# Kernel optimization log

Hardware: AMD Instinct MI355X
Metric: run time of the kernel (lower is better)

## Reference

```python
import jax, jax.numpy as jnp
import numpy as np

B, H, S, D = 4, 16, 2048, 128

def setup_inputs() -> dict:
    key = jax.random.key(0)
    kk, kq, kv = jax.random.split(key, 3)
    k = jax.random.normal(kk, (B, H, S, D), dtype=jnp.float32)
    q = jax.random.normal(kq, (B, H, S, D), dtype=jnp.float32)
    v = jax.random.normal(kv, (B, H, S, D), dtype=jnp.float32)
    # causal mask: True = masked out (strictly upper triangle)
    mask = jnp.triu(jnp.ones((S, S), dtype=bool), k=1)
    return {"k": k, "q": q, "v": v, "mask": mask}

def reference(k, q, v, mask):
    d_k = k.shape[-1]
    # scores: [B, H, S, S]
    scores = jnp.einsum("bhqd,bhkd->bhqk", q, k) / jnp.sqrt(jnp.asarray(d_k, q.dtype))
    scores = jnp.where(mask, -jnp.inf, scores)
    # numerically stable softmax over last dim (matches manual max/exp/sum)
    p = jax.nn.softmax(scores, axis=-1)
    return jnp.einsum("bhqk,bhkd->bhqd", p, v)
```

## Files before the change

kernel.cpp:

```cpp
#include <hip/hip_runtime.h>
#include <hip/hip_bf16.h>
#include <math.h>

#define BATCH 4
#define HEADS 16
#define SEQ   2048
#define DIM   128
#define BHN   (BATCH*HEADS)

#define BQ 128
#define WQ 32
#define KT 32
#define NXB (SEQ/BQ)

typedef short bf16x8 __attribute__((ext_vector_type(8)));
typedef float f32x4  __attribute__((ext_vector_type(4)));

static __device__ __forceinline__ unsigned short f2bf(float f) {
    union { float f; unsigned u; } x; x.f = f;
    unsigned r = x.u + 0x7FFF + ((x.u >> 16) & 1);
    return (unsigned short)(r >> 16);
}

static __device__ __forceinline__ void async_cp16(const unsigned short* g, unsigned short* l) {
    __builtin_amdgcn_global_load_lds(
        (const __attribute__((address_space(1))) unsigned int*)g,
        (__attribute__((address_space(3))) unsigned int*)l,
        16, 0, 0);
}

__global__ __launch_bounds__(256) void cvt_kv(
    const float* __restrict__ k, const float* __restrict__ v,
    unsigned short* __restrict__ kb, unsigned short* __restrict__ vt) {
    __shared__ unsigned short T[DIM][72];
    const int bh = blockIdx.y;
    const int s0 = blockIdx.x * 64;
    const int t  = threadIdx.x;
    const long rbase = ((long)bh * SEQ + s0) * DIM;

    #pragma unroll
    for (int u = 0; u < 2; ++u) {
        long e = rbase + (long)(t + u * 256) * 16;
        const float* src = k + e;
        unsigned short* dst = kb + e;
        #pragma unroll
        for (int h = 0; h < 2; ++h) {
            float4 a0 = *(const float4*)(src + h * 8);
            float4 a1 = *(const float4*)(src + h * 8 + 4);
            union { uint4 u4; unsigned short s[8]; } p;
            p.s[0]=f2bf(a0.x); p.s[1]=f2bf(a0.y); p.s[2]=f2bf(a0.z); p.s[3]=f2bf(a0.w);
            p.s[4]=f2bf(a1.x); p.s[5]=f2bf(a1.y); p.s[6]=f2bf(a1.z); p.s[7]=f2bf(a1.w);
            *(uint4*)(dst + h * 8) = p.u4;
        }
    }
    {
        const int r = t >> 2, i = t & 3;
        const float* src = v + rbase + (long)r * DIM + i * 32;
        #pragma unroll
        for (int j = 0; j < 8; ++j) {
            float4 x = *(const float4*)(src + j * 4);
            const int d = i * 32 + j * 4;
            T[d + 0][r] = f2bf(x.x); T[d + 1][r] = f2bf(x.y);
            T[d + 2][r] = f2bf(x.z); T[d + 3][r] = f2bf(x.w);
        }
    }
    __syncthreads();
    {
        const int d = t >> 1, h = t & 1;
        unsigned short* dst = vt + ((long)bh * DIM + d) * SEQ + s0 + h * 32;
        #pragma unroll
        for (int m = 0; m < 4; ++m)
            *(uint4*)(dst + m * 8) = *(const uint4*)&T[d][h * 32 + m * 8];
    }
}

__global__ __launch_bounds__(256, 2) void attn_fwd(
    const float* __restrict__ qg,
    const unsigned short* __restrict__ kb,
    const unsigned short* __restrict__ vtg,
    float* __restrict__ out) {

    __shared__ unsigned short Kt[2][KT][DIM];
    __shared__ unsigned short Vt[2][DIM][KT];
    __shared__ unsigned short Pl[4][2][16][KT + 8];

    const int tid  = threadIdx.x;
    const int w    = tid >> 6;
    const int lane = tid & 63;
    const int quad = lane >> 4;
    const int ql   = lane & 15;

    const int flat = blockIdx.x;
    const int xcd  = flat & 7;
    const int slot = flat >> 3;
    const int bh   = (xcd << 3) | (slot & 7);
    const int shi  = slot >> 3;
    const int xb   = (shi < 4) ? (15 - shi)
                   : (shi < 8) ? (shi - 4)
                   : (shi < 12) ? shi
                   : (19 - shi);
    const int qb0 = xb * BQ;
    const int qw0 = qb0 + w * WQ;

    const long base = (long)bh * SEQ * DIM;
    const float scale = 0.08838834764831845f * 1.4426950408889634f;

    bf16x8 qf[2][4];
    #pragma unroll
    for (int mb = 0; mb < 2; ++mb) {
        const float* qr = qg + base + (long)(qw0 + mb * 16 + ql) * DIM;
        #pragma unroll
        for (int c = 0; c < 4; ++c) {
            const float* p = qr + c * 32 + quad * 8;
            float4 x = *(const float4*)(p);
            float4 y = *(const float4*)(p + 4);
            union { bf16x8 v; unsigned short s[8]; } u;
            u.s[0]=f2bf(x.x*scale); u.s[1]=f2bf(x.y*scale);
            u.s[2]=f2bf(x.z*scale); u.s[3]=f2bf(x.w*scale);
            u.s[4]=f2bf(y.x*scale); u.s[5]=f2bf(y.y*scale);
            u.s[6]=f2bf(y.z*scale); u.s[7]=f2bf(y.w*scale);
            qf[mb][c] = u.v;
        }
    }

    f32x4 acc[2][8];
    #pragma unroll
    for (int mb = 0; mb < 2; ++mb)
        #pragma unroll
        for (int n = 0; n < 8; ++n)
            acc[mb][n] = (f32x4){0.f, 0.f, 0.f, 0.f};

    float m_[2] = {-INFINITY, -INFINITY};
    float l_[2] = {0.f, 0.f};

    auto stage = [&](int buf, int k0) {
        #pragma unroll
        for (int i = 0; i < 2; ++i) {
            const int idx = tid + i * 256;
            const int r   = idx >> 4;
            const int chg = (idx & 15) ^ (r & 15);
            async_cp16(kb + base + (long)(k0 + r) * DIM + chg * 8,
                       &Kt[buf][0][0] + ((tid >> 6) * 64 + i * 256) * 8);
            const int d   = idx >> 2;
            const int cvg = (idx & 3) ^ ((d >> 1) & 3);
            async_cp16(vtg + base + (long)d * SEQ + k0 + cvg * 8,
                       &Vt[buf][0][0] + ((tid >> 6) * 64 + i * 256) * 8);
        }
    };

    const int ntile = (qb0 + BQ) / KT;

    stage(0, 0);

    for (int t = 0; t < ntile; ++t) {
        const int buf = t & 1;
        const int k0  = t * KT;
        __syncthreads();

        if (t + 1 < ntile) stage(buf ^ 1, k0 + KT);

        const bool active = (k0 < qw0 + WQ);
        if (active) {
            f32x4 sacc[2][2];
            #pragma unroll
            for (int mb = 0; mb < 2; ++mb)
                #pragma unroll
                for (int kk = 0; kk < 2; ++kk)
                    sacc[mb][kk] = (f32x4){0.f, 0.f, 0.f, 0.f};
            #pragma unroll
            for (int c = 0; c < 4; ++c) {
                const int sw = ((c * 4 + quad) ^ ql) * 8;
                bf16x8 kf0 = *(const bf16x8*)&Kt[buf][ql]     [sw];
                bf16x8 kf1 = *(const bf16x8*)&Kt[buf][16 + ql][sw];
                #pragma unroll
                for (int mb = 0; mb < 2; ++mb) {
                    sacc[mb][0] = __builtin_amdgcn_mfma_f32_16x16x32_bf16(kf0, qf[mb][c], sacc[mb][0], 0, 0, 0);
                    sacc[mb][1] = __builtin_amdgcn_mfma_f32_16x16x32_bf16(kf1, qf[mb][c], sacc[mb][1], 0, 0, 0);
                }
            }

            bf16x8 vf[8];
            #pragma unroll
            for (int n = 0; n < 8; ++n)
                vf[n] = *(const bf16x8*)&Vt[buf][n * 16 + ql][(quad ^ ((ql >> 1) & 3)) * 8];

            float alpha_[2];
            bool  resc_[2];
            #pragma unroll
            for (int mb = 0; mb < 2; ++mb) {
                const int qrow   = qw0 + mb * 16 + ql;
                const bool needm = (k0 + KT - 1 > qw0 + mb * 16);
                float s[2][4];
                float tmax = -INFINITY;
                #pragma unroll
                for (int kk = 0; kk < 2; ++kk)
                    #pragma unroll
                    for (int r = 0; r < 4; ++r) {
                        float sv = sacc[mb][kk][r];
                        if (needm) {
                            int kg = k0 + kk * 16 + quad * 4 + r;
                            sv = (kg <= qrow) ? sv : -INFINITY;
                        }
                        s[kk][r] = sv;
                        tmax = fmaxf(tmax, sv);
                    }
                tmax = fmaxf(tmax, __shfl_xor(tmax, 16));
                tmax = fmaxf(tmax, __shfl_xor(tmax, 32));

                const bool skip = __all(tmax <= m_[mb] + 8.0f);
                const float mnew = skip ? m_[mb] : fmaxf(m_[mb], tmax);

                float rsum = 0.f;
                #pragma unroll
                for (int kk = 0; kk < 2; ++kk) {
                    float p0 = __builtin_amdgcn_exp2f(s[kk][0] - mnew);
                    float p1 = __builtin_amdgcn_exp2f(s[kk][1] - mnew);
                    float p2 = __builtin_amdgcn_exp2f(s[kk][2] - mnew);
                    float p3 = __builtin_amdgcn_exp2f(s[kk][3] - mnew);
                    rsum += (p0 + p1) + (p2 + p3);
                    union { uint2 u; __hip_bfloat162 h[2]; } pu;
                    pu.h[0] = __float22bfloat162_rn(float2{p0, p1});
                    pu.h[1] = __float22bfloat162_rn(float2{p2, p3});
                    *(uint2*)&Pl[w][mb][ql][kk * 16 + quad * 4] = pu.u;
                }
                rsum += __shfl_xor(rsum, 16);
                rsum += __shfl_xor(rsum, 32);

                if (skip) {
                    l_[mb] += rsum;
                    alpha_[mb] = 1.f; resc_[mb] = false;
                } else {
                    const float al = __builtin_amdgcn_exp2f(m_[mb] - mnew);
                    l_[mb] = l_[mb] * al + rsum;
                    m_[mb] = mnew;
                    alpha_[mb] = al; resc_[mb] = true;
                }
            }

            bf16x8 pf0 = *(const bf16x8*)&Pl[w][0][ql][quad * 8];
            bf16x8 pf1 = *(const bf16x8*)&Pl[w][1][ql][quad * 8];

            #pragma unroll
            for (int mb = 0; mb < 2; ++mb) {
                if (resc_[mb]) {
                    #pragma unroll
                    for (int r = 0; r < 4; ++r) {
                        float ar = __shfl(alpha_[mb], quad * 4 + r);
                        #pragma unroll
                        for (int n = 0; n < 8; ++n) acc[mb][n][r] *= ar;
                    }
                }
                const bf16x8 pf = mb ? pf1 : pf0;
                #pragma unroll
                for (int n = 0; n < 8; ++n)
                    acc[mb][n] = __builtin_amdgcn_mfma_f32_16x16x32_bf16(pf, vf[n], acc[mb][n], 0, 0, 0);
            }
        }
    }

    #pragma unroll
    for (int mb = 0; mb < 2; ++mb) {
        #pragma unroll
        for (int r = 0; r < 4; ++r) {
            float lr = __shfl(l_[mb], quad * 4 + r);
            float il = 1.0f / lr;
            long orow = base + (long)(qw0 + mb * 16 + quad * 4 + r) * DIM;
            #pragma unroll
            for (int n = 0; n < 8; ++n)
                out[orow + n * 16 + ql] = acc[mb][n][r] * il;
        }
    }
}

extern "C" void kernel_launch(void* const* d_in, const int* in_sizes, int n_in,
                              void* d_out, int out_size, void* d_ws, size_t ws_size,
                              hipStream_t stream) {
    const float* k = (const float*)d_in[0];
    const float* q = (const float*)d_in[1];
    const float* v = (const float*)d_in[2];
    float* o = (float*)d_out;

    unsigned short* kb = (unsigned short*)d_ws;
    unsigned short* vt = kb + (size_t)BHN * SEQ * DIM;

    cvt_kv<<<dim3(SEQ / 64, BHN), dim3(256), 0, stream>>>(k, v, kb, vt);

    attn_fwd<<<dim3(NXB * BHN), dim3(256), 0, stream>>>(q, kb, vt, o);
}
```

Before: 352.4 us.

## Rework KV conversion, raise occupancy, unroll loop by two with setprio

The V transpose in the conversion kernel now goes through registers instead of shared memory, and bf16 packing uses the paired conversion intrinsic. The attention kernel raises its launch-bounds occupancy hint from 2 to 3 blocks per CU and precomputes staging and LDS fragment offsets. It unrolls the tile loop by two so buffer indices are compile-time constants, wraps the MFMA sections in s_setprio, and tightens the lazy-rescale threshold from 8 to 4. The occupancy hint caps registers per thread and could cause spills, and the smaller threshold makes rescaling happen more often.

Result: slower. 414.9 us (+17.7%).

```diff
diff --git a/kernel.cpp b/kernel.cpp
--- a/kernel.cpp
+++ b/kernel.cpp
@@ -32,7 +32,6 @@
 __global__ __launch_bounds__(256) void cvt_kv(
     const float* __restrict__ k, const float* __restrict__ v,
     unsigned short* __restrict__ kb, unsigned short* __restrict__ vt) {
-    __shared__ unsigned short T[DIM][72];
     const int bh = blockIdx.y;
     const int s0 = blockIdx.x * 64;
     const int t  = threadIdx.x;
@@ -47,34 +46,38 @@
         for (int h = 0; h < 2; ++h) {
             float4 a0 = *(const float4*)(src + h * 8);
             float4 a1 = *(const float4*)(src + h * 8 + 4);
-            union { uint4 u4; unsigned short s[8]; } p;
-            p.s[0]=f2bf(a0.x); p.s[1]=f2bf(a0.y); p.s[2]=f2bf(a0.z); p.s[3]=f2bf(a0.w);
-            p.s[4]=f2bf(a1.x); p.s[5]=f2bf(a1.y); p.s[6]=f2bf(a1.z); p.s[7]=f2bf(a1.w);
-            *(uint4*)(dst + h * 8) = p.u4;
+            union { uint4 q; __hip_bfloat162 b[4]; } p;
+            p.b[0] = __float22bfloat162_rn(float2{a0.x, a0.y});
+            p.b[1] = __float22bfloat162_rn(float2{a0.z, a0.w});
+            p.b[2] = __float22bfloat162_rn(float2{a1.x, a1.y});
+            p.b[3] = __float22bfloat162_rn(float2{a1.z, a1.w});
+            *(uint4*)(dst + h * 8) = p.q;
         }
     }
     {
-        const int r = t >> 2, i = t & 3;
-        const float* src = v + rbase + (long)r * DIM + i * 32;
-        #pragma unroll
-        for (int j = 0; j < 8; ++j) {
-            float4 x = *(const float4*)(src + j * 4);
-            const int d = i * 32 + j * 4;
-            T[d + 0][r] = f2bf(x.x); T[d + 1][r] = f2bf(x.y);
-            T[d + 2][r] = f2bf(x.z); T[d + 3][r] = f2bf(x.w);
-        }
-    }
-    __syncthreads();
-    {
-        const int d = t >> 1, h = t & 1;
-        unsigned short* dst = vt + ((long)bh * DIM + d) * SEQ + s0 + h * 32;
-        #pragma unroll
-        for (int m = 0; m < 4; ++m)
-            *(uint4*)(dst + m * 8) = *(const uint4*)&T[d][h * 32 + m * 8];
-    }
-}
-
-__global__ __launch_bounds__(256, 2) void attn_fwd(
+        const int rg = t & 15;
+        const int dg = t >> 4;
+        const float* src = v + rbase + (long)(rg * 4) * DIM + dg * 8;
+        float a[4][8];
+        #pragma unroll
+        for (int rr = 0; rr < 4; ++rr) {
+            float4 x = *(const float4*)(src + rr * DIM);
+            float4 y = *(const float4*)(src + rr * DIM + 4);
+            a[rr][0]=x.x; a[rr][1]=x.y; a[rr][2]=x.z; a[rr][3]=x.w;
+            a[rr][4]=y.x; a[rr][5]=y.y; a[rr][6]=y.z; a[rr][7]=y.w;
+        }
+        unsigned short* dstb = vt + ((long)bh * DIM + dg * 8) * SEQ + s0 + rg * 4;
+        #pragma unroll
+        for (int dd = 0; dd < 8; ++dd) {
+            union { uint2 u; __hip_bfloat162 b[2]; } p;
+            p.b[0] = __float22bfloat162_rn(float2{a[0][dd], a[1][dd]});
+            p.b[1] = __float22bfloat162_rn(float2{a[2][dd], a[3][dd]});
+            *(uint2*)(dstb + (long)dd * SEQ) = p.u;
+        }
+    }
+}
+
+__global__ __launch_bounds__(256, 3) void attn_fwd(
     const float* __restrict__ qg,
     const unsigned short* __restrict__ kb,
     const unsigned short* __restrict__ vtg,
@@ -133,129 +136,156 @@
     float m_[2] = {-INFINITY, -INFINITY};
     float l_[2] = {0.f, 0.f};
 
-    auto stage = [&](int buf, int k0) {
+    int koff[2], voff[2];
+    #pragma unroll
+    for (int i = 0; i < 2; ++i) {
+        const int idx = tid + i * 256;
+        const int r   = idx >> 4;
+        const int chg = (idx & 15) ^ (r & 15);
+        koff[i] = r * DIM + chg * 8;
+        const int d   = idx >> 2;
+        const int cvg = (idx & 3) ^ ((d >> 1) & 3);
+        voff[i] = d * SEQ + cvg * 8;
+    }
+    const int ldso = ((tid >> 6) * 64) * 8;
+    const unsigned short* kbb = kb + base;
+    const unsigned short* vbb = vtg + base;
+
+    auto stage = [&](int buf, int k0s) {
+        const unsigned short* ku = kbb + k0s * DIM;
+        const unsigned short* vu = vbb + k0s;
         #pragma unroll
         for (int i = 0; i < 2; ++i) {
-            const int idx = tid + i * 256;
-            const int r   = idx >> 4;
-            const int chg = (idx & 15) ^ (r & 15);
-            async_cp16(kb + base + (long)(k0 + r) * DIM + chg * 8,
-                       &Kt[buf][0][0] + ((tid >> 6) * 64 + i * 256) * 8);
-            const int d   = idx >> 2;
-            const int cvg = (idx & 3) ^ ((d >> 1) & 3);
-            async_cp16(vtg + base + (long)d * SEQ + k0 + cvg * 8,
-                       &Vt[buf][0][0] + ((tid >> 6) * 64 + i * 256) * 8);
+            async_cp16(ku + koff[i], &Kt[buf][0][0] + ldso + i * 2048);
+            async_cp16(vu + voff[i], &Vt[buf][0][0] + ldso + i * 2048);
         }
     };
 
-    const int ntile = (qb0 + BQ) / KT;
-
-    stage(0, 0);
-
-    for (int t = 0; t < ntile; ++t) {
-        const int buf = t & 1;
-        const int k0  = t * KT;
-        __syncthreads();
-
-        if (t + 1 < ntile) stage(buf ^ 1, k0 + KT);
-
-        const bool active = (k0 < qw0 + WQ);
-        if (active) {
-            f32x4 sacc[2][2];
-            #pragma unroll
-            for (int mb = 0; mb < 2; ++mb)
+    const unsigned short* kfb[4];
+    #pragma unroll
+    for (int c = 0; c < 4; ++c)
+        kfb[c] = &Kt[0][ql][((c * 4 + quad) ^ ql) * 8];
+    const unsigned short* vfb = &Vt[0][0][0] + ql * KT + (quad ^ ((ql >> 1) & 3)) * 8;
+    unsigned short*       pwb = &Pl[0][0][0][0] + w * (2 * 16 * (KT + 8)) + ql * (KT + 8);
+    const unsigned short* prb = pwb + quad * 8;
+    const int PMB = 16 * (KT + 8);
+
+    auto body = [&](const int buf, const int k0) {
+        if (k0 >= qw0 + WQ) return;
+        const int kbo = buf * (KT * DIM);
+        const int vbo = buf * (DIM * KT);
+
+        f32x4 sacc[2][2];
+        #pragma unroll
+        for (int mb = 0; mb < 2; ++mb)
+            #pragma unroll
+            for (int kk = 0; kk < 2; ++kk)
+                sacc[mb][kk] = (f32x4){0.f, 0.f, 0.f, 0.f};
+        __builtin_amdgcn_s_setprio(1);
+        #pragma unroll
+        for (int c = 0; c < 4; ++c) {
+            bf16x8 kf0 = *(const bf16x8*)(kfb[c] + kbo);
+            bf16x8 kf1 = *(const bf16x8*)(kfb[c] + kbo + 16 * DIM);
+            #pragma unroll
+            for (int mb = 0; mb < 2; ++mb) {
+                sacc[mb][0] = __builtin_amdgcn_mfma_f32_16x16x32_bf16(kf0, qf[mb][c], sacc[mb][0], 0, 0, 0);
+                sacc[mb][1] = __builtin_amdgcn_mfma_f32_16x16x32_bf16(kf1, qf[mb][c], sacc[mb][1], 0, 0, 0);
+            }
+        }
+        __builtin_amdgcn_s_setprio(0);
+
+        bf16x8 vf[8];
+        #pragma unroll
+        for (int n = 0; n < 8; ++n)
+            vf[n] = *(const bf16x8*)(vfb + vbo + n * (16 * KT));
+
+        float alpha_[2];
+        bool  resc_[2];
+        #pragma unroll
+        for (int mb = 0; mb < 2; ++mb) {
+            const int qrow   = qw0 + mb * 16 + ql;
+            const bool needm = (k0 + KT - 1 > qw0 + mb * 16);
+            float s[2][4];
+            float tmax = -INFINITY;
+            #pragma unroll
+            for (int kk = 0; kk < 2; ++kk)
                 #pragma unroll
-                for (int kk = 0; kk < 2; ++kk)
-                    sacc[mb][kk] = (f32x4){0.f, 0.f, 0.f, 0.f};
-            #pragma unroll
-            for (int c = 0; c < 4; ++c) {
-                const int sw = ((c * 4 + quad) ^ ql) * 8;
-                bf16x8 kf0 = *(const bf16x8*)&Kt[buf][ql]     [sw];
-                bf16x8 kf1 = *(const bf16x8*)&Kt[buf][16 + ql][sw];
+                for (int r = 0; r < 4; ++r) {
+                    float sv = sacc[mb][kk][r];
+                    if (needm) {
+                        int kg = k0 + kk * 16 + quad * 4 + r;
+                        sv = (kg <= qrow) ? sv : -INFINITY;
+                    }
+                    s[kk][r] = sv;
+                    tmax = fmaxf(tmax, sv);
+                }
+            tmax = fmaxf(tmax, __shfl_xor(tmax, 16));
+            tmax = fmaxf(tmax, __shfl_xor(tmax, 32));
+
+            const bool skip = __all(tmax <= m_[mb] + 4.0f);
+            const float mnew = skip ? m_[mb] : fmaxf(m_[mb], tmax);
+
+            float rsum = 0.f;
+            #pragma unroll
+            for (int kk = 0; kk < 2; ++kk) {
+                float p0 = __builtin_amdgcn_exp2f(s[kk][0] - mnew);
+                float p1 = __builtin_amdgcn_exp2f(s[kk][1] - mnew);
+                float p2 = __builtin_amdgcn_exp2f(s[kk][2] - mnew);
+                float p3 = __builtin_amdgcn_exp2f(s[kk][3] - mnew);
+                rsum += (p0 + p1) + (p2 + p3);
+                union { uint2 u; __hip_bfloat162 h[2]; } pu;
+                pu.h[0] = __float22bfloat162_rn(float2{p0, p1});
+                pu.h[1] = __float22bfloat162_rn(float2{p2, p3});
+                *(uint2*)(pwb + mb * PMB + kk * 16 + quad * 4) = pu.u;
+            }
+            rsum += __shfl_xor(rsum, 16);
+            rsum += __shfl_xor(rsum, 32);
+
+            if (skip) {
+                l_[mb] += rsum;
+                alpha_[mb] = 1.f; resc_[mb] = false;
+            } else {
+                const float al = __builtin_amdgcn_exp2f(m_[mb] - mnew);
+                l_[mb] = l_[mb] * al + rsum;
+                m_[mb] = mnew;
+                alpha_[mb] = al; resc_[mb] = true;
+            }
+        }
+
+        bf16x8 pf0 = *(const bf16x8*)(prb);
+        bf16x8 pf1 = *(const bf16x8*)(prb + PMB);
+
+        #pragma unroll
+        for (int mb = 0; mb < 2; ++mb) {
+            if (resc_[mb]) {
                 #pragma unroll
-                for (int mb = 0; mb < 2; ++mb) {
-                    sacc[mb][0] = __builtin_amdgcn_mfma_f32_16x16x32_bf16(kf0, qf[mb][c], sacc[mb][0], 0, 0, 0);
-                    sacc[mb][1] = __builtin_amdgcn_mfma_f32_16x16x32_bf16(kf1, qf[mb][c], sacc[mb][1], 0, 0, 0);
+                for (int r = 0; r < 4; ++r) {
+                    float ar = __shfl(alpha_[mb], quad * 4 + r);
+                    #pragma unroll
+                    for (int n = 0; n < 8; ++n) acc[mb][n][r] *= ar;
                 }
             }
-
-            bf16x8 vf[8];
+            const bf16x8 pf = mb ? pf1 : pf0;
+            __builtin_amdgcn_s_setprio(1);
             #pragma unroll
             for (int n = 0; n < 8; ++n)
-                vf[n] = *(const bf16x8*)&Vt[buf][n * 16 + ql][(quad ^ ((ql >> 1) & 3)) * 8];
-
-            float alpha_[2];
-            bool  resc_[2];
-            #pragma unroll
-            for (int mb = 0; mb < 2; ++mb) {
-                const int qrow   = qw0 + mb * 16 + ql;
-                const bool needm = (k0 + KT - 1 > qw0 + mb * 16);
-                float s[2][4];
-                float tmax = -INFINITY;
-                #pragma unroll
-                for (int kk = 0; kk < 2; ++kk)
-                    #pragma unroll
-                    for (int r = 0; r < 4; ++r) {
-                        float sv = sacc[mb][kk][r];
-                        if (needm) {
-                            int kg = k0 + kk * 16 + quad * 4 + r;
-                            sv = (kg <= qrow) ? sv : -INFINITY;
-                        }
-                        s[kk][r] = sv;
-                        tmax = fmaxf(tmax, sv);
-                    }
-                tmax = fmaxf(tmax, __shfl_xor(tmax, 16));
-                tmax = fmaxf(tmax, __shfl_xor(tmax, 32));
-
-                const bool skip = __all(tmax <= m_[mb] + 8.0f);
-                const float mnew = skip ? m_[mb] : fmaxf(m_[mb], tmax);
-
-                float rsum = 0.f;
-                #pragma unroll
-                for (int kk = 0; kk < 2; ++kk) {
-                    float p0 = __builtin_amdgcn_exp2f(s[kk][0] - mnew);
-                    float p1 = __builtin_amdgcn_exp2f(s[kk][1] - mnew);
-                    float p2 = __builtin_amdgcn_exp2f(s[kk][2] - mnew);
-                    float p3 = __builtin_amdgcn_exp2f(s[kk][3] - mnew);
-                    rsum += (p0 + p1) + (p2 + p3);
-                    union { uint2 u; __hip_bfloat162 h[2]; } pu;
-                    pu.h[0] = __float22bfloat162_rn(float2{p0, p1});
-                    pu.h[1] = __float22bfloat162_rn(float2{p2, p3});
-                    *(uint2*)&Pl[w][mb][ql][kk * 16 + quad * 4] = pu.u;
-                }
-                rsum += __shfl_xor(rsum, 16);
-                rsum += __shfl_xor(rsum, 32);
-
-                if (skip) {
-                    l_[mb] += rsum;
-                    alpha_[mb] = 1.f; resc_[mb] = false;
-                } else {
-                    const float al = __builtin_amdgcn_exp2f(m_[mb] - mnew);
-                    l_[mb] = l_[mb] * al + rsum;
-                    m_[mb] = mnew;
-                    alpha_[mb] = al; resc_[mb] = true;
-                }
-            }
-
-            bf16x8 pf0 = *(const bf16x8*)&Pl[w][0][ql][quad * 8];
-            bf16x8 pf1 = *(const bf16x8*)&Pl[w][1][ql][quad * 8];
-
-            #pragma unroll
-            for (int mb = 0; mb < 2; ++mb) {
-                if (resc_[mb]) {
-                    #pragma unroll
-                    for (int r = 0; r < 4; ++r) {
-                        float ar = __shfl(alpha_[mb], quad * 4 + r);
-                        #pragma unroll
-                        for (int n = 0; n < 8; ++n) acc[mb][n][r] *= ar;
-                    }
-                }
-                const bf16x8 pf = mb ? pf1 : pf0;
-                #pragma unroll
-                for (int n = 0; n < 8; ++n)
-                    acc[mb][n] = __builtin_amdgcn_mfma_f32_16x16x32_bf16(pf, vf[n], acc[mb][n], 0, 0, 0);
-            }
-        }
+                acc[mb][n] = __builtin_amdgcn_mfma_f32_16x16x32_bf16(pf, vf[n], acc[mb][n], 0, 0, 0);
+            __builtin_amdgcn_s_setprio(0);
+        }
+    };
+
+    const int ntile = 4 * xb + 4;
+
+    stage(0, 0);
+
+    for (int tt = 0; tt < ntile; tt += 2) {
+        __syncthreads();
+        stage(1, (tt + 1) * KT);
+        body(0, tt * KT);
+
+        __syncthreads();
+        if (tt + 2 < ntile) stage(0, (tt + 2) * KT);
+        body(1, (tt + 1) * KT);
     }
 
     #pragma unroll
```
